# Performance work log

Hardware: AMD Instinct MI355X
Metric: run time of the kernel (lower is better)

The kernel has to match this reference:

```python
import jax, jax.numpy as jnp
import numpy as np

L, D, H, HK, DH, F, V, T, B = 8, 1024, 16, 4, 64, 2816, 32000, 1024, 2
G = H // HK
THETA = 10000.0
EPS = 1e-6
SCALE = DH ** -0.5


def _rope_tables(t, dh, theta):
    inv = 1.0 / theta ** (jnp.arange(0, dh, 2, dtype=jnp.float32) / dh)  # [dh/2]
    ang = jnp.arange(t, dtype=jnp.float32)[:, None] * inv[None, :]       # [T, dh/2]
    return jnp.cos(ang), jnp.sin(ang)


def _apply_rope(x, cos, sin):
    # x: [B, T, h, DH] -> rotate pairs (even, odd)
    xr = x.reshape(*x.shape[:-1], DH // 2, 2)
    x0, x1 = xr[..., 0], xr[..., 1]
    c = cos[None, :, None, :]
    s = sin[None, :, None, :]
    out = jnp.stack([x0 * c - x1 * s, x0 * s + x1 * c], axis=-1)
    return out.reshape(*x.shape)


def _rmsnorm(x, w):
    var = jnp.mean(x * x, axis=-1, keepdims=True)
    return x * jax.lax.rsqrt(var + EPS) * w


def setup_inputs() -> dict:
    key = jax.random.key(0)
    ks = jax.random.split(key, 10)
    s = 0.02
    return {
        "ids": jax.random.randint(ks[0], (B, T), 0, V),
        "emb": jax.random.normal(ks[1], (V, D), jnp.float32) * s,
        "qw": jax.random.normal(ks[2], (L, H * DH, D), jnp.float32) * s,
        "kw": jax.random.normal(ks[3], (L, HK * DH, D), jnp.float32) * s,
        "vw": jax.random.normal(ks[4], (L, HK * DH, D), jnp.float32) * s,
        "ow": jax.random.normal(ks[5], (L, D, D), jnp.float32) * s,
        "w1": jax.random.normal(ks[6], (L, F, D), jnp.float32) * s,
        "w2": jax.random.normal(ks[7], (L, D, F), jnp.float32) * s,
        "w3": jax.random.normal(ks[8], (L, F, D), jnp.float32) * s,
        "n1": jnp.ones((L, D), jnp.float32),
        "n2": jnp.ones((L, D), jnp.float32),
        "nf": jnp.ones((D,), jnp.float32),
    }


def _forward(ids, emb, qw, kw, vw, ow, w1, w2, w3, n1, n2, nf):
    cos, sin = _rope_tables(T, DH, THETA)
    causal = jnp.tril(jnp.ones((T, T), dtype=bool))  # [T, T]
    x = emb[ids]  # [B, T, D]
    for l in range(L):
        xn = _rmsnorm(x, n1[l])
        q = jnp.einsum("btd,ed->bte", xn, qw[l]).reshape(B, T, H, DH)
        k = jnp.einsum("btd,ed->bte", xn, kw[l]).reshape(B, T, HK, DH)
        v = jnp.einsum("btd,ed->bte", xn, vw[l]).reshape(B, T, HK, DH)
        q = _apply_rope(q, cos, sin)
        k = _apply_rope(k, cos, sin)
        # GQA: group query heads over shared kv heads
        qg = q.transpose(0, 2, 1, 3).reshape(B, HK, G, T, DH)
        kh = k.transpose(0, 2, 1, 3)  # [B, HK, T, DH]
        vh = v.transpose(0, 2, 1, 3)
        scores = jnp.einsum("bkgtd,bksd->bkgts", qg, kh) * SCALE
        scores = jnp.where(causal, scores, -jnp.inf)
        p = jax.nn.softmax(scores, axis=-1)
        out = jnp.einsum("bkgts,bksd->bkgtd", p, vh)
        out = out.reshape(B, H, T, DH).transpose(0, 2, 1, 3).reshape(B, T, D)
        x = x + jnp.einsum("btd,ed->bte", out, ow[l])
        xn2 = _rmsnorm(x, n2[l])
        h1 = jnp.einsum("btd,fd->btf", xn2, w1[l])
        h3 = jnp.einsum("btd,fd->btf", xn2, w3[l])
        x = x + jnp.einsum("btf,df->btd", jax.nn.silu(h1) * h3, w2[l])
    x = _rmsnorm(x, nf)
    logits = jnp.einsum("btd,vd->btv", x, emb)  # tied lm_head
    return logits


def reference(ids, emb, qw, kw, vw, ow, w1, w2, w3, n1, n2, nf):
    return _forward(ids, emb, qw, kw, vw, ow, w1, w2, w3, n1, n2, nf)
```

## Files before the change

### kernel.cpp

```cpp
#include <hip/hip_runtime.h>
#include <math.h>

#define L_ 8
#define D_ 1024
#define H_ 16
#define HK_ 4
#define DH_ 64
#define F_ 2816
#define V_ 32000
#define T_ 1024
#define B_ 2
#define M_ (B_*T_)
#define SCALE_ 0.125f

typedef unsigned short u16;
typedef unsigned int   u32;
typedef __attribute__((ext_vector_type(4))) float  f32x4;
typedef __attribute__((ext_vector_type(8))) short  bf16x8;
typedef __attribute__((ext_vector_type(4))) unsigned short u16x4;
typedef __attribute__((ext_vector_type(4))) unsigned int   u32x4;

__device__ __forceinline__ float bf2f(u16 h) {
    union { u32 u; float f; } v; v.u = ((u32)h) << 16; return v.f;
}
__device__ __forceinline__ u16 f2bf(float f) {
    union { float f; u32 u; } v; v.f = f;
    u32 r = v.u + 0x7fffu + ((v.u >> 16) & 1u);
    return (u16)(r >> 16);
}

__device__ __forceinline__ void gl_lds16(const void* g, void* l) {
    __builtin_amdgcn_global_load_lds(
        (const __attribute__((address_space(1))) unsigned int*)g,
        (__attribute__((address_space(3))) unsigned int*)l,
        16, 0, 0);
}

template<int BM, int BN, int EPI>
__global__ __launch_bounds__(256)
void gemm2_k(const u16* __restrict__ A, int K,
             const u16* __restrict__ W, int N,
             float* __restrict__ Of, u16* __restrict__ Ob,
             const float* __restrict__ tc, const float* __restrict__ ts)
{
    constexpr int FM = BM / 32;
    constexpr int FN = BN / 32;
    constexpr int GM = M_ / BM;
    constexpr int IPA = BM / 64;
    constexpr int IPB = BN / 64;
    __shared__ u16 sA[2 * BM * 32];
    __shared__ u16 sB[2 * BN * 32];

    const int tid  = threadIdx.x;
    const int lane = tid & 63, wv = tid >> 6;
    const int wm = wv >> 1, wn = wv & 1;
    const int l15 = lane & 15, lhi = lane >> 4;
    const int m0 = wm * (BM / 2), n0 = wn * (BN / 2);

    const int nwg = gridDim.x;
    const int q8 = nwg >> 3, r8 = nwg & 7;
    const int xcd = blockIdx.x & 7, off8 = blockIdx.x >> 3;
    const int wgid = (xcd < r8 ? xcd * (q8 + 1) : r8 * (q8 + 1) + (xcd - r8) * q8) + off8;
    const int tM = wgid % GM, tN = wgid / GM;

    const int srow = lane >> 2;
    const int scol = (lane & 3) * 8;

    const u16* Abase = A + (size_t)(tM * BM) * K;
    const u16* Wbase = W + (size_t)(tN * BN) * K;

    f32x4 acc[FM][FN];
#pragma unroll
    for (int i = 0; i < FM; ++i)
#pragma unroll
        for (int j = 0; j < FN; ++j) acc[i][j] = f32x4{0.f, 0.f, 0.f, 0.f};

    auto stage = [&](int kt, int buf) {
        u16* sa = sA + buf * (BM * 32);
        u16* sb = sB + buf * (BN * 32);
#pragma unroll
        for (int i = 0; i < IPA; ++i) {
            int c = wv * IPA + i;
            gl_lds16(Abase + (size_t)(c * 16 + srow) * K + kt + scol, sa + c * 512);
        }
#pragma unroll
        for (int i = 0; i < IPB; ++i) {
            int c = wv * IPB + i;
            gl_lds16(Wbase + (size_t)(c * 16 + srow) * K + kt + scol, sb + c * 512);
        }
    };

    const int nt = K >> 5;
    stage(0, 0);
    asm volatile("s_waitcnt vmcnt(0)" ::: "memory");
    __syncthreads();

    int cur = 0;
    for (int t = 0; t < nt; ++t) {
        if (t + 1 < nt) stage((t + 1) << 5, cur ^ 1);

        const u16* sa = sA + cur * (BM * 32);
        const u16* sb = sB + cur * (BN * 32);
        bf16x8 av[FM], bv[FN];
#pragma unroll
        for (int i = 0; i < FM; ++i)
            av[i] = *(const bf16x8*)&sa[(m0 + i * 16 + l15) * 32 + lhi * 8];
#pragma unroll
        for (int j = 0; j < FN; ++j)
            bv[j] = *(const bf16x8*)&sb[(n0 + j * 16 + l15) * 32 + lhi * 8];
#pragma unroll
        for (int i = 0; i < FM; ++i)
#pragma unroll
            for (int j = 0; j < FN; ++j)
                acc[i][j] = __builtin_amdgcn_mfma_f32_16x16x32_bf16(
                    av[i], bv[j], acc[i][j], 0, 0, 0);

        if (t + 1 < nt) {
            asm volatile("s_waitcnt vmcnt(0)" ::: "memory");
            __syncthreads();
            cur ^= 1;
        }
    }

#pragma unroll
    for (int i = 0; i < FM; ++i)
#pragma unroll
        for (int j = 0; j < FN; ++j) {
            size_t gm = (size_t)tM * BM + m0 + i * 16 + lhi * 4;
            size_t gn = (size_t)tN * BN + n0 + j * 16 + l15;
#pragma unroll
            for (int r = 0; r < 4; ++r) {
                float v = acc[i][j][r];
                size_t idx = (gm + r) * (size_t)N + gn;
                if (EPI == 0) {
                    Ob[idx] = f2bf(v);
                } else if (EPI == 1) {
                    Of[idx] = v;
                } else if (EPI == 2) {
                    Of[idx] += v;
                } else if (EPI == 3) {
                    float b = __shfl_xor(v, 1);
                    if ((lane & 1) == 0) {
                        float s = v / (1.0f + expf(-v));
                        Ob[(gm + r) * (size_t)F_ + (gn >> 1)] = f2bf(s * b);
                    }
                } else {
                    float b = __shfl_xor(v, 1);
                    int gni = (int)gn;
                    int gmr = (int)(gm + r);
                    if (gni < 1280) {
                        int dd = gni & 63;
                        int jj = dd >> 1;
                        int tt = gmr & (T_ - 1);
                        float c = tc[tt * 32 + jj], s = ts[tt * 32 + jj];
                        float ro = ((dd & 1) == 0) ? (v * c - b * s) : (b * s + v * c);
                        Ob[idx] = f2bf(ro);
                    } else {
                        int vc = gni - 1280;
                        int hk = vc >> 6, dd = vc & 63;
                        int bb = gmr >> 10, tt = gmr & (T_ - 1);
                        ((u16*)Of)[((size_t)((bb * HK_ + hk) * DH_ + dd)) * T_ + tt] = f2bf(v);
                    }
                }
            }
        }
}

__global__ __launch_bounds__(256)
void cvt_k(const float* __restrict__ src, u16* __restrict__ dst,
           unsigned long long sStride, unsigned long long dStride)
{
    int l = blockIdx.y;
    size_t i = ((size_t)blockIdx.x * 256 + threadIdx.x) * 4;
    f32x4 v = *(const f32x4*)(src + l * sStride + i);
    u16x4 o;
    o.x = f2bf(v.x); o.y = f2bf(v.y); o.z = f2bf(v.z); o.w = f2bf(v.w);
    *(u16x4*)(dst + l * dStride + i) = o;
}

__global__ __launch_bounds__(256)
void cvt_il_k(const float* __restrict__ src, u16* __restrict__ dst,
              unsigned long long sStride, unsigned long long dStride, int off)
{
    int f = blockIdx.x, l = blockIdx.y;
    int i = threadIdx.x * 4;
    f32x4 v = *(const f32x4*)(src + l * sStride + (size_t)f * D_ + i);
    u16x4 o;
    o.x = f2bf(v.x); o.y = f2bf(v.y); o.z = f2bf(v.z); o.w = f2bf(v.w);
    *(u16x4*)(dst + l * dStride + (size_t)(2 * f + off) * D_ + i) = o;
}

template<int BM, int BN, int EPI, int NW>
__global__ __launch_bounds__(256)
void gemm_k(const u16* __restrict__ A, int K,
            const float* __restrict__ W0, const float* __restrict__ W1p,
            const float* __restrict__ W2p, int N0, int N1, int N,
            float* __restrict__ Of, u16* __restrict__ Ob)
{
    constexpr int FM = BM / 32;
    constexpr int FN = BN / 32;
    constexpr int LS = 40;
    __shared__ u16 sA[BM * LS];
    __shared__ u16 sB[BN * LS];

    const int tid  = threadIdx.x;
    const int lane = tid & 63, wv = tid >> 6;
    const int wm = wv >> 1, wn = wv & 1;
    const int l15 = lane & 15, lhi = lane >> 4;
    const int m0 = wm * (BM / 2), n0 = wn * (BN / 2);
    const int tM = blockIdx.y, tN = blockIdx.x;

    f32x4 acc[FM][FN];
#pragma unroll
    for (int i = 0; i < FM; ++i)
#pragma unroll
        for (int j = 0; j < FN; ++j) acc[i][j] = f32x4{0.f, 0.f, 0.f, 0.f};

    for (int kt = 0; kt < K; kt += 32) {
#pragma unroll
        for (int i = 0; i < BM / 64; ++i) {
            int cid = tid + i * 256;
            int row = cid >> 2, kc = cid & 3;
            const u16* src = A + (size_t)(tM * BM + row) * K + kt + kc * 8;
            *(u32x4*)&sA[row * LS + kc * 8] = *(const u32x4*)src;
        }
#pragma unroll
        for (int i = 0; i < BN / 32; ++i) {
            int cid = tid + i * 256;
            int row = cid >> 3, kc = cid & 7;
            int n = tN * BN + row;
            const float* wr;
            if (NW == 1)      wr = W0 + (size_t)n * K;
            else if (NW == 2) wr = (n < N0) ? (W0 + (size_t)n * K)
                                            : (W1p + (size_t)(n - N0) * K);
            else              wr = (n < N0) ? (W0 + (size_t)n * K)
                               : (n < N0 + N1) ? (W1p + (size_t)(n - N0) * K)
                                               : (W2p + (size_t)(n - N0 - N1) * K);
            f32x4 v = *(const f32x4*)(wr + kt + kc * 4);
            u16x4 o;
            o.x = f2bf(v.x); o.y = f2bf(v.y); o.z = f2bf(v.z); o.w = f2bf(v.w);
            *(u16x4*)&sB[row * LS + kc * 4] = o;
        }
        __syncthreads();

        bf16x8 av[FM], bv[FN];
#pragma unroll
        for (int i = 0; i < FM; ++i)
            av[i] = *(const bf16x8*)&sA[(m0 + i * 16 + l15) * LS + lhi * 8];
#pragma unroll
        for (int j = 0; j < FN; ++j)
            bv[j] = *(const bf16x8*)&sB[(n0 + j * 16 + l15) * LS + lhi * 8];
#pragma unroll
        for (int i = 0; i < FM; ++i)
#pragma unroll
            for (int j = 0; j < FN; ++j)
                acc[i][j] = __builtin_amdgcn_mfma_f32_16x16x32_bf16(
                    av[i], bv[j], acc[i][j], 0, 0, 0);
        __syncthreads();
    }

#pragma unroll
    for (int i = 0; i < FM; ++i)
#pragma unroll
        for (int j = 0; j < FN; ++j) {
            size_t gm = (size_t)tM * BM + m0 + i * 16 + lhi * 4;
            size_t gn = (size_t)tN * BN + n0 + j * 16 + l15;
#pragma unroll
            for (int r = 0; r < 4; ++r) {
                float v = acc[i][j][r];
                size_t idx = (gm + r) * (size_t)N + gn;
                if (EPI == 0)      Ob[idx] = f2bf(v);
                else if (EPI == 1) Of[idx] = v;
                else               Of[idx] += v;
            }
        }
}

__global__ __launch_bounds__(512)
void attn3_k(const u16* __restrict__ qkv, const u16* __restrict__ vt,
             u16* __restrict__ attn)
{
    const int qt = 31 - blockIdx.x;
    const int hk = blockIdx.y, b = blockIdx.z;
    const int tid = threadIdx.x;
    const int lane = tid & 63, w = tid >> 6;
    const int l15 = lane & 15, lhi = lane >> 4;
    const int h = hk * 4 + (w & 3);
    const int rg = w >> 2;

    __shared__ u16 sK[128 * 64];
    __shared__ u16 sVT[64 * 128];
    __shared__ u16 sP[8][16 * 136];

    const int q0 = qt * 32;
    const int qr0 = q0 + rg * 16;
    const u16* qptr = qkv + (size_t)(b * T_ + qr0 + l15) * 1536 + h * 64 + lhi * 8;
    bf16x8 aq0 = *(const bf16x8*)qptr;
    bf16x8 aq1 = *(const bf16x8*)(qptr + 32);

    f32x4 accO[4];
#pragma unroll
    for (int d = 0; d < 4; ++d) accO[d] = f32x4{0.f, 0.f, 0.f, 0.f};
    float m_r[4] = {-1e30f, -1e30f, -1e30f, -1e30f};
    float l_r[4] = {0.f, 0.f, 0.f, 0.f};
    const int myq = qr0 + lhi * 4;
    const int qmaxw = qr0 + 15;
    u16* sPw = sP[w];

    const int ntiles = (qt >> 2) + 1;
    const u16* vtb = vt + (size_t)((b * HK_ + hk) * DH_) * T_;
    const int L = lane;

    for (int kt = 0; kt < ntiles; ++kt) {
        const int t0 = kt * 128;
#pragma unroll
        for (int i = 0; i < 2; ++i) {
            int c = w * 2 + i;
            int row = c * 8 + (L >> 3);
            int p = L & 7;
            const u16* src = qkv + (size_t)(b * T_ + t0 + row) * 1536 + 1024 + hk * 64
                             + ((p ^ (row & 7)) * 8);
            gl_lds16(src, sK + c * 512);
        }
#pragma unroll
        for (int i = 0; i < 2; ++i) {
            int c = w * 2 + i;
            int row = c * 4 + (L >> 4);
            int p = L & 15;
            const u16* src = vtb + (size_t)row * T_ + t0 + ((p ^ (row & 15)) * 8);
            gl_lds16(src, sVT + c * 512);
        }
        asm volatile("s_waitcnt vmcnt(0)" ::: "memory");
        __syncthreads();

        const bool lastt = (kt == ntiles - 1);

        f32x4 accS[8];
#pragma unroll
        for (int nf = 0; nf < 8; ++nf)
            accS[nf] = f32x4{-1e30f, -1e30f, -1e30f, -1e30f};
#pragma unroll
        for (int pk = 0; pk < 4; ++pk) {
            if (t0 + pk * 32 > qmaxw) continue;
            f32x4 s0 = f32x4{0.f, 0.f, 0.f, 0.f};
            f32x4 s1 = f32x4{0.f, 0.f, 0.f, 0.f};
#pragma unroll
            for (int kk = 0; kk < 2; ++kk) {
                bf16x8 aqs = kk ? aq1 : aq0;
                int r0 = (pk * 2) * 16 + l15;
                int r1 = (pk * 2 + 1) * 16 + l15;
                int ls = kk * 4 + lhi;
                bf16x8 b0 = *(const bf16x8*)&sK[r0 * 64 + ((ls ^ (r0 & 7)) * 8)];
                bf16x8 b1 = *(const bf16x8*)&sK[r1 * 64 + ((ls ^ (r1 & 7)) * 8)];
                s0 = __builtin_amdgcn_mfma_f32_16x16x32_bf16(aqs, b0, s0, 0, 0, 0);
                s1 = __builtin_amdgcn_mfma_f32_16x16x32_bf16(aqs, b1, s1, 0, 0, 0);
            }
#pragma unroll
            for (int r = 0; r < 4; ++r) {
                float v0 = s0[r] * SCALE_;
                float v1 = s1[r] * SCALE_;
                if (lastt) {
                    int kp0 = t0 + (pk * 2) * 16 + l15;
                    int kp1 = kp0 + 16;
                    if (kp0 > myq + r) v0 = -1e30f;
                    if (kp1 > myq + r) v1 = -1e30f;
                }
                accS[pk * 2][r] = v0;
                accS[pk * 2 + 1][r] = v1;
            }
        }

        float sc[4];
#pragma unroll
        for (int r = 0; r < 4; ++r) {
            float mx = accS[0][r];
#pragma unroll
            for (int nf = 1; nf < 8; ++nf) mx = fmaxf(mx, accS[nf][r]);
#pragma unroll
            for (int off = 1; off < 16; off <<= 1) mx = fmaxf(mx, __shfl_xor(mx, off));
            float mn = fmaxf(m_r[r], mx);
            sc[r] = expf(m_r[r] - mn);
            m_r[r] = mn;
        }
        float rs[4] = {0.f, 0.f, 0.f, 0.f};
#pragma unroll
        for (int pk = 0; pk < 4; ++pk) {
            if (t0 + pk * 32 > qmaxw) continue;
#pragma unroll
            for (int g = 0; g < 2; ++g) {
                int nf = pk * 2 + g;
#pragma unroll
                for (int r = 0; r < 4; ++r) {
                    float p = expf(accS[nf][r] - m_r[r]);
                    accS[nf][r] = p;
                    rs[r] += p;
                }
            }
        }
#pragma unroll
        for (int r = 0; r < 4; ++r) {
#pragma unroll
            for (int off = 1; off < 16; off <<= 1) rs[r] += __shfl_xor(rs[r], off);
            l_r[r] = l_r[r] * sc[r] + rs[r];
        }
#pragma unroll
        for (int d = 0; d < 4; ++d)
#pragma unroll
            for (int r = 0; r < 4; ++r) accO[d][r] *= sc[r];

#pragma unroll
        for (int pk = 0; pk < 4; ++pk) {
            if (t0 + pk * 32 > qmaxw) continue;
#pragma unroll
            for (int g = 0; g < 2; ++g) {
                int nf = pk * 2 + g;
#pragma unroll
                for (int r = 0; r < 4; ++r)
                    sPw[(lhi * 4 + r) * 136 + nf * 16 + l15] = f2bf(accS[nf][r]);
            }
        }

#pragma unroll
        for (int kk = 0; kk < 4; ++kk) {
            if (t0 + kk * 32 > qmaxw) continue;
            bf16x8 pas = *(const bf16x8*)&sPw[l15 * 136 + kk * 32 + lhi * 8];
#pragma unroll
            for (int nf = 0; nf < 4; ++nf) {
                int row = nf * 16 + l15;
                int ls = kk * 4 + lhi;
                bf16x8 bvv = *(const bf16x8*)&sVT[row * 128 + ((ls ^ (row & 15)) * 8)];
                accO[nf] = __builtin_amdgcn_mfma_f32_16x16x32_bf16(pas, bvv, accO[nf], 0, 0, 0);
            }
        }
        __syncthreads();
    }

#pragma unroll
    for (int d = 0; d < 4; ++d)
#pragma unroll
        for (int r = 0; r < 4; ++r) {
            int row = qr0 + lhi * 4 + r;
            float o = accO[d][r] / l_r[r];
            attn[(size_t)(b * T_ + row) * 1024 + h * 64 + d * 16 + l15] = f2bf(o);
        }
}

__global__ __launch_bounds__(256)
void attn_k(const u16* __restrict__ qkv, u16* __restrict__ attn)
{
    const int qt = blockIdx.x, h = blockIdx.y, b = blockIdx.z;
    const int hk = h >> 2;
    const int tid = threadIdx.x;
    const int lane = tid & 63, w = tid >> 6;
    const int l15 = lane & 15, lhi = lane >> 4;
    __shared__ u16 sK[64 * 72];
    __shared__ u16 sVT[64 * 74];
    __shared__ u16 sP[4 * 16 * 72];

    const int q0 = qt * 64;
    const u16* qptr = qkv + (size_t)(b * T_ + q0 + w * 16 + l15) * 1536 + h * 64 + lhi * 8;
    bf16x8 aq0 = *(const bf16x8*)qptr;
    bf16x8 aq1 = *(const bf16x8*)(qptr + 32);

    f32x4 accO[4];
#pragma unroll
    for (int d = 0; d < 4; ++d) accO[d] = f32x4{0.f, 0.f, 0.f, 0.f};
    float m_r[4] = {-1e30f, -1e30f, -1e30f, -1e30f};
    float l_r[4] = {0.f, 0.f, 0.f, 0.f};
    const int myq = q0 + w * 16 + lhi * 4;
    u16* sPw = sP + w * 16 * 72;

    for (int kt = 0; kt <= qt; ++kt) {
#pragma unroll
        for (int i = 0; i < 2; ++i) {
            int cid = tid + i * 256;
            int r = cid >> 3, kc = cid & 7;
            const u16* src = qkv + (size_t)(b * T_ + kt * 64 + r) * 1536 + 1024 + hk * 64 + kc * 8;
            *(u32x4*)&sK[r * 72 + kc * 8] = *(const u32x4*)src;
        }
#pragma unroll
        for (int i = 0; i < 2; ++i) {
            int cid = tid + i * 256;
            int tt = cid >> 3, dc = cid & 7;
            const u16* src = qkv + (size_t)(b * T_ + kt * 64 + tt) * 1536 + 1280 + hk * 64 + dc * 8;
            bf16x8 vv = *(const bf16x8*)src;
#pragma unroll
            for (int j = 0; j < 8; ++j) sVT[(dc * 8 + j) * 74 + tt] = (u16)vv[j];
        }
        __syncthreads();

        f32x4 accS[4];
#pragma unroll
        for (int nf = 0; nf < 4; ++nf) accS[nf] = f32x4{0.f, 0.f, 0.f, 0.f};
#pragma unroll
        for (int s = 0; s < 2; ++s) {
            bf16x8 aqs = s ? aq1 : aq0;
#pragma unroll
            for (int nf = 0; nf < 4; ++nf) {
                bf16x8 bk = *(const bf16x8*)&sK[(nf * 16 + l15) * 72 + s * 32 + lhi * 8];
                accS[nf] = __builtin_amdgcn_mfma_f32_16x16x32_bf16(aqs, bk, accS[nf], 0, 0, 0);
            }
        }
#pragma unroll
        for (int nf = 0; nf < 4; ++nf)
#pragma unroll
            for (int r = 0; r < 4; ++r) {
                float v = accS[nf][r] * SCALE_;
                if (kt == qt) {
                    int kp = kt * 64 + nf * 16 + l15;
                    if (kp > myq + r) v = -1e30f;
                }
                accS[nf][r] = v;
            }
        float sc[4];
#pragma unroll
        for (int r = 0; r < 4; ++r) {
            float mx = fmaxf(fmaxf(accS[0][r], accS[1][r]), fmaxf(accS[2][r], accS[3][r]));
#pragma unroll
            for (int off = 1; off < 16; off <<= 1) mx = fmaxf(mx, __shfl_xor(mx, off));
            float mn = fmaxf(m_r[r], mx);
            sc[r] = expf(m_r[r] - mn);
            m_r[r] = mn;
        }
        float rs[4] = {0.f, 0.f, 0.f, 0.f};
#pragma unroll
        for (int nf = 0; nf < 4; ++nf)
#pragma unroll
            for (int r = 0; r < 4; ++r) {
                float p = expf(accS[nf][r] - m_r[r]);
                accS[nf][r] = p;
                rs[r] += p;
            }
#pragma unroll
        for (int r = 0; r < 4; ++r) {
#pragma unroll
            for (int off = 1; off < 16; off <<= 1) rs[r] += __shfl_xor(rs[r], off);
            l_r[r] = l_r[r] * sc[r] + rs[r];
        }
#pragma unroll
        for (int d = 0; d < 4; ++d)
#pragma unroll
            for (int r = 0; r < 4; ++r) accO[d][r] *= sc[r];

#pragma unroll
        for (int nf = 0; nf < 4; ++nf)
#pragma unroll
            for (int r = 0; r < 4; ++r)
                sPw[(lhi * 4 + r) * 72 + nf * 16 + l15] = f2bf(accS[nf][r]);
        bf16x8 pa0 = *(const bf16x8*)&sPw[l15 * 72 + lhi * 8];
        bf16x8 pa1 = *(const bf16x8*)&sPw[l15 * 72 + 32 + lhi * 8];
#pragma unroll
        for (int s = 0; s < 2; ++s) {
            bf16x8 pas = s ? pa1 : pa0;
#pragma unroll
            for (int d = 0; d < 4; ++d) {
                bf16x8 bvv = *(const bf16x8*)&sVT[(d * 16 + l15) * 74 + s * 32 + lhi * 8];
                accO[d] = __builtin_amdgcn_mfma_f32_16x16x32_bf16(pas, bvv, accO[d], 0, 0, 0);
            }
        }
        __syncthreads();
    }

#pragma unroll
    for (int d = 0; d < 4; ++d)
#pragma unroll
        for (int r = 0; r < 4; ++r) {
            int row = q0 + w * 16 + lhi * 4 + r;
            float o = accO[d][r] / l_r[r];
            attn[(size_t)(b * T_ + row) * 1024 + h * 64 + d * 16 + l15] = f2bf(o);
        }
}

__global__ __launch_bounds__(256)
void gather_k(const int* __restrict__ ids, const float* __restrict__ emb,
              float* __restrict__ x)
{
    int m = blockIdx.x, tid = threadIdx.x;
    int id = ids[m];
    *(f32x4*)(x + (size_t)m * D_ + tid * 4) =
        *(const f32x4*)(emb + (size_t)id * D_ + tid * 4);
}

__global__ __launch_bounds__(256)
void rmsnorm_k(const float* __restrict__ x, const float* __restrict__ g,
               u16* __restrict__ out)
{
    const int row = blockIdx.x, tid = threadIdx.x;
    const float* xr = x + (size_t)row * D_;
    f32x4 v = *(const f32x4*)(xr + tid * 4);
    float ss = v.x * v.x + v.y * v.y + v.z * v.z + v.w * v.w;
#pragma unroll
    for (int off = 32; off >= 1; off >>= 1) ss += __shfl_xor(ss, off);
    __shared__ float red[4];
    if ((tid & 63) == 0) red[tid >> 6] = ss;
    __syncthreads();
    float tot = red[0] + red[1] + red[2] + red[3];
    float rr = rsqrtf(tot * (1.0f / D_) + 1e-6f);
    f32x4 wv = *(const f32x4*)(g + tid * 4);
    u16x4 o;
    o.x = f2bf(v.x * rr * wv.x); o.y = f2bf(v.y * rr * wv.y);
    o.z = f2bf(v.z * rr * wv.z); o.w = f2bf(v.w * rr * wv.w);
    *(u16x4*)(out + (size_t)row * D_ + tid * 4) = o;
}

__global__ __launch_bounds__(256)
void rope_tab_k(float* __restrict__ tc, float* __restrict__ ts)
{
    int idx = blockIdx.x * 256 + threadIdx.x;
    int t = idx >> 5, j = idx & 31;
    float inv = powf(10000.0f, -(float)j * (1.0f / 32.0f));
    float ang = (float)t * inv;
    tc[idx] = cosf(ang);
    ts[idx] = sinf(ang);
}

__global__ __launch_bounds__(256)
void silu_f32_k(const float* __restrict__ h13, u16* __restrict__ hh)
{
    int m = blockIdx.y;
    int f = blockIdx.x * 256 + threadIdx.x;
    float a = h13[(size_t)m * (2 * F_) + f];
    float c = h13[(size_t)m * (2 * F_) + F_ + f];
    float s = a / (1.0f + expf(-a));
    hh[(size_t)m * F_ + f] = f2bf(s * c);
}

__global__ __launch_bounds__(640)
void rope_slow_k(u16* __restrict__ qkv)
{
    int m = blockIdx.x;
    int c2 = threadIdx.x;
    int col = (c2 < 512) ? (c2 * 2) : (1024 + (c2 - 512) * 2);
    int d = col & 63;
    int t = m & (T_ - 1);
    float ang = (float)t * powf(10000.0f, -(float)d / 64.0f);
    float cs = cosf(ang), sn = sinf(ang);
    u16* p = qkv + (size_t)m * 1536 + col;
    float x0 = bf2f(p[0]), x1 = bf2f(p[1]);
    p[0] = f2bf(x0 * cs - x1 * sn);
    p[1] = f2bf(x0 * sn + x1 * cs);
}

extern "C" void kernel_launch(void* const* d_in, const int* in_sizes, int n_in,
                              void* d_out, int out_size, void* d_ws, size_t ws_size,
                              hipStream_t stream)
{
    const int*   ids = (const int*)d_in[0];
    const float* emb = (const float*)d_in[1];
    const float* qw  = (const float*)d_in[2];
    const float* kw  = (const float*)d_in[3];
    const float* vw  = (const float*)d_in[4];
    const float* ow  = (const float*)d_in[5];
    const float* w1  = (const float*)d_in[6];
    const float* w2  = (const float*)d_in[7];
    const float* w3  = (const float*)d_in[8];
    const float* n1  = (const float*)d_in[9];
    const float* n2  = (const float*)d_in[10];
    const float* nfw = (const float*)d_in[11];
    float* out = (float*)d_out;
    char*  ws  = (char*)d_ws;

    float* x    = (float*)(ws);
    u16*   xn   = (u16*)(ws + 8388608ULL);
    u16*   qkvb = (u16*)(ws + 12582912ULL);
    u16*   attnb= (u16*)(ws + 18874368ULL);
    u16*   hh   = (u16*)(ws + 46137344ULL);
    float* ropec= (float*)(ws + 57671680ULL);
    float* ropes= (float*)(ws + 57802752ULL);
    u16*   embb = (u16*)(ws + 57933824ULL);
    u16*   wqkv = (u16*)(ws + 123469824ULL);
    u16*   wob  = (u16*)(ws + 148635648ULL);
    u16*   w13b = (u16*)(ws + 165412864ULL);
    u16*   w2b  = (u16*)(ws + 257687552ULL);
    u16*   vtb  = (u16*)(ws + 303824896ULL);
    const unsigned long long NEED = 304873472ULL;

    if (ws_size >= NEED) {
        cvt_k<<<dim3(32000, 1), 256, 0, stream>>>(emb, embb, 0, 0);
        cvt_k<<<dim3(1024, L_), 256, 0, stream>>>(qw, wqkv,            1048576ULL, 1572864ULL);
        cvt_k<<<dim3(256,  L_), 256, 0, stream>>>(kw, wqkv + 1048576,  262144ULL,  1572864ULL);
        cvt_k<<<dim3(256,  L_), 256, 0, stream>>>(vw, wqkv + 1310720,  262144ULL,  1572864ULL);
        cvt_k<<<dim3(1024, L_), 256, 0, stream>>>(ow, wob,             1048576ULL, 1048576ULL);
        cvt_il_k<<<dim3(2816, L_), 256, 0, stream>>>(w1, w13b, 2883584ULL, 5767168ULL, 0);
        cvt_il_k<<<dim3(2816, L_), 256, 0, stream>>>(w3, w13b, 2883584ULL, 5767168ULL, 1);
        cvt_k<<<dim3(2816, L_), 256, 0, stream>>>(w2, w2b,             2883584ULL, 2883584ULL);
        rope_tab_k<<<T_ * 32 / 256, 256, 0, stream>>>(ropec, ropes);

        gather_k<<<M_, 256, 0, stream>>>(ids, emb, x);

        for (int l = 0; l < L_; ++l) {
            rmsnorm_k<<<M_, 256, 0, stream>>>(x, n1 + l * D_, xn);
            gemm2_k<64, 64, 4><<<32 * 24, 256, 0, stream>>>(
                xn, D_, wqkv + (size_t)l * 1572864, 1536, (float*)vtb, qkvb, ropec, ropes);
            attn3_k<<<dim3(32, HK_, B_), 512, 0, stream>>>(qkvb, vtb, attnb);
            gemm2_k<64, 64, 2><<<32 * 16, 256, 0, stream>>>(
                attnb, D_, wob + (size_t)l * 1048576, 1024, x, nullptr, nullptr, nullptr);
            rmsnorm_k<<<M_, 256, 0, stream>>>(x, n2 + l * D_, xn);
            gemm2_k<128, 128, 3><<<16 * 44, 256, 0, stream>>>(
                xn, D_, w13b + (size_t)l * 5767168, 5632, nullptr, hh, nullptr, nullptr);
            gemm2_k<64, 64, 2><<<32 * 16, 256, 0, stream>>>(
                hh, F_, w2b + (size_t)l * 2883584, 1024, x, nullptr, nullptr, nullptr);
        }

        rmsnorm_k<<<M_, 256, 0, stream>>>(x, nfw, xn);
        gemm2_k<128, 128, 1><<<16 * 250, 256, 0, stream>>>(
            xn, D_, embb, V_, out, nullptr, nullptr, nullptr);
        return;
    }

    float* h13f = (float*)(ws + 23068672ULL);
    u16*   hhf  = (u16*)(ws + 69206016ULL);
    gather_k<<<M_, 256, 0, stream>>>(ids, emb, x);

    for (int l = 0; l < L_; ++l) {
        rmsnorm_k<<<M_, 256, 0, stream>>>(x, n1 + l * D_, xn);
        gemm_k<128, 64, 0, 3><<<dim3(24, 16), 256, 0, stream>>>(
            xn, D_,
            qw + (size_t)l * H_ * DH_ * D_,
            kw + (size_t)l * HK_ * DH_ * D_,
            vw + (size_t)l * HK_ * DH_ * D_,
            1024, 256, 1536, nullptr, qkvb);
        rope_slow_k<<<M_, 640, 0, stream>>>(qkvb);
        attn_k<<<dim3(T_ / 64, H_, B_), 256, 0, stream>>>(qkvb, attnb);
        gemm_k<128, 64, 2, 1><<<dim3(16, 16), 256, 0, stream>>>(
            attnb, D_, ow + (size_t)l * D_ * D_, nullptr, nullptr,
            0, 0, D_, x, nullptr);
        rmsnorm_k<<<M_, 256, 0, stream>>>(x, n2 + l * D_, xn);
        gemm_k<128, 128, 1, 2><<<dim3(44, 16), 256, 0, stream>>>(
            xn, D_, w1 + (size_t)l * F_ * D_, w3 + (size_t)l * F_ * D_, nullptr,
            F_, 0, 2 * F_, h13f, nullptr);
        silu_f32_k<<<dim3(11, M_), 256, 0, stream>>>(h13f, hhf);
        gemm_k<128, 64, 2, 1><<<dim3(16, 16), 256, 0, stream>>>(
            hhf, F_, w2 + (size_t)l * D_ * F_, nullptr, nullptr,
            0, 0, D_, x, nullptr);
    }

    rmsnorm_k<<<M_, 256, 0, stream>>>(x, nfw, xn);
    gemm_k<128, 128, 1, 1><<<dim3(250, 16), 256, 0, stream>>>(
        xn, D_, emb, nullptr, nullptr, 0, 0, V_, out, nullptr);
}
```

Baseline: 1.807 ms.

## Add 256x256-tile 8-wave GEMM kernel for FFN up-projection and LM head

Adds a new 512-thread GEMM kernel with 256x256 output tiles, XOR-swizzled LDS staging via direct global-to-LDS loads, a double-buffered A/B pipeline with loads spread across sub-phases, XCD-aware block remapping, and raised wave priority around MFMA bursts. It replaces the 128x128 gemm2_k for the fused W1/W3 SwiGLU projection and the tied LM-head projection. The aim is more reuse per loaded tile and better overlap of memory with MFMA work. In exchange it uses a large LDS footprint and many accumulators, and launches far fewer workgroups (176 for the FFN), which may underfill the GPU.

```diff
diff --git a/kernel.cpp b/kernel.cpp
--- a/kernel.cpp
+++ b/kernel.cpp
@@ -34,6 +34,149 @@
         (const __attribute__((address_space(1))) unsigned int*)g,
         (__attribute__((address_space(3))) unsigned int*)l,
         16, 0, 0);
+}
+
+__device__ __forceinline__ void bar8() {
+    asm volatile("" ::: "memory");
+    __builtin_amdgcn_s_barrier();
+    asm volatile("" ::: "memory");
+}
+
+template<int EPI>
+__global__ __launch_bounds__(512)
+void gemm8_k(const u16* __restrict__ A, int K,
+             const u16* __restrict__ W, int N,
+             float* __restrict__ Of, u16* __restrict__ Ob)
+{
+    constexpr int TS = 256 * 64;
+    __shared__ u16 sA[2 * TS];
+    __shared__ u16 sB[2 * TS];
+
+    const int tid = threadIdx.x;
+    const int lane = tid & 63, wv = tid >> 6;
+    const int wm = wv >> 2, wn = wv & 3;
+    const int l15 = lane & 15, lhi = lane >> 4;
+
+    const int nwg = gridDim.x;
+    const int q8 = nwg >> 3;
+    const int xcd = blockIdx.x & 7, off8 = blockIdx.x >> 3;
+    const int wgid = xcd * q8 + off8;
+    const int tM = wgid & 7, tN = wgid >> 3;
+
+    const u16* Abase = A + (size_t)(tM * 256) * K;
+    const u16* Wbase = W + (size_t)(tN * 256) * K;
+
+    const int srow8 = lane >> 3;
+    const int sp    = lane & 7;
+    const int scol  = (sp ^ srow8) * 8;
+
+    auto stage = [&](const u16* gbase, int t2, int h, u16* dst) {
+        const u16* g = gbase + (size_t)(h * 128) * K + (t2 << 6);
+        u16* d = dst + h * 8192;
+#pragma unroll
+        for (int i = 0; i < 2; ++i) {
+            int c = wv * 2 + i;
+            int row = c * 8 + srow8;
+            gl_lds16(g + (size_t)row * K + scol, d + c * 512);
+        }
+    };
+
+    f32x4 acc[8][4];
+#pragma unroll
+    for (int i = 0; i < 8; ++i)
+#pragma unroll
+        for (int j = 0; j < 4; ++j) acc[i][j] = f32x4{0.f, 0.f, 0.f, 0.f};
+
+    const int nt = K >> 6;
+    stage(Abase, 0, 0, sA); stage(Abase, 0, 1, sA);
+    stage(Wbase, 0, 0, sB); stage(Wbase, 0, 1, sB);
+    if (nt > 1) {
+        stage(Wbase, 1, 0, sB + TS); stage(Wbase, 1, 1, sB + TS);
+        asm volatile("s_waitcnt vmcnt(4)" ::: "memory");
+    } else {
+        asm volatile("s_waitcnt vmcnt(0)" ::: "memory");
+    }
+    bar8();
+
+    for (int t = 0; t < nt; ++t) {
+        const int cur = t & 1;
+        const u16* sa = sA + cur * TS;
+        const u16* sb = sB + cur * TS;
+        u16* saN = sA + (cur ^ 1) * TS;
+        u16* sbN = sB + cur * TS;
+
+        bf16x8 breg[4][2];
+
+#pragma unroll
+        for (int p = 0; p < 4; ++p) {
+            if (p == 0) {
+#pragma unroll
+                for (int j = 0; j < 4; ++j)
+#pragma unroll
+                    for (int kk = 0; kk < 2; ++kk) {
+                        int br = wn * 64 + j * 16 + l15;
+                        int ls = kk * 4 + lhi;
+                        breg[j][kk] = *(const bf16x8*)
+                            &sb[br * 64 + ((ls ^ (br & 7)) * 8)];
+                    }
+            }
+            bf16x8 areg[2][2];
+#pragma unroll
+            for (int mi = 0; mi < 2; ++mi)
+#pragma unroll
+                for (int kk = 0; kk < 2; ++kk) {
+                    int ar = wm * 128 + (p * 2 + mi) * 16 + l15;
+                    int ls = kk * 4 + lhi;
+                    areg[mi][kk] = *(const bf16x8*)
+                        &sa[ar * 64 + ((ls ^ (ar & 7)) * 8)];
+                }
+
+            if (p == 0 && t + 1 < nt) stage(Abase, t + 1, 0, saN);
+            if (p == 1 && t + 1 < nt) stage(Abase, t + 1, 1, saN);
+            if (p == 2 && t + 2 < nt) stage(Wbase, t + 2, 0, sbN);
+            if (p == 3 && t + 2 < nt) stage(Wbase, t + 2, 1, sbN);
+
+            if (p == 3 && t + 1 < nt) {
+                if (t + 2 < nt) asm volatile("s_waitcnt vmcnt(4)" ::: "memory");
+                else            asm volatile("s_waitcnt vmcnt(0)" ::: "memory");
+            }
+
+            bar8();
+            asm volatile("s_waitcnt lgkmcnt(0)" ::: "memory");
+            __builtin_amdgcn_s_setprio(1);
+#pragma unroll
+            for (int mi = 0; mi < 2; ++mi)
+#pragma unroll
+                for (int j = 0; j < 4; ++j)
+#pragma unroll
+                    for (int kk = 0; kk < 2; ++kk)
+                        acc[p * 2 + mi][j] = __builtin_amdgcn_mfma_f32_16x16x32_bf16(
+                            areg[mi][kk], breg[j][kk], acc[p * 2 + mi][j], 0, 0, 0);
+            __builtin_amdgcn_s_setprio(0);
+            bar8();
+        }
+    }
+
+#pragma unroll
+    for (int i = 0; i < 8; ++i)
+#pragma unroll
+        for (int j = 0; j < 4; ++j) {
+            size_t gm = (size_t)tM * 256 + wm * 128 + i * 16 + lhi * 4;
+            size_t gn = (size_t)tN * 256 + wn * 64 + j * 16 + l15;
+#pragma unroll
+            for (int r = 0; r < 4; ++r) {
+                float v = acc[i][j][r];
+                if (EPI == 1) {
+                    Of[(gm + r) * (size_t)N + gn] = v;
+                } else {
+                    float b = __shfl_xor(v, 1);
+                    if ((lane & 1) == 0) {
+                        float s = v / (1.0f + expf(-v));
+                        Ob[(gm + r) * (size_t)F_ + (gn >> 1)] = f2bf(s * b);
+                    }
+                }
+            }
+        }
 }
 
 template<int BM, int BN, int EPI>
@@ -696,15 +839,15 @@
             gemm2_k<64, 64, 2><<<32 * 16, 256, 0, stream>>>(
                 attnb, D_, wob + (size_t)l * 1048576, 1024, x, nullptr, nullptr, nullptr);
             rmsnorm_k<<<M_, 256, 0, stream>>>(x, n2 + l * D_, xn);
-            gemm2_k<128, 128, 3><<<16 * 44, 256, 0, stream>>>(
-                xn, D_, w13b + (size_t)l * 5767168, 5632, nullptr, hh, nullptr, nullptr);
+            gemm8_k<3><<<8 * 22, 512, 0, stream>>>(
+                xn, D_, w13b + (size_t)l * 5767168, 5632, nullptr, hh);
             gemm2_k<64, 64, 2><<<32 * 16, 256, 0, stream>>>(
                 hh, F_, w2b + (size_t)l * 2883584, 1024, x, nullptr, nullptr, nullptr);
         }
 
         rmsnorm_k<<<M_, 256, 0, stream>>>(x, nfw, xn);
-        gemm2_k<128, 128, 1><<<16 * 250, 256, 0, stream>>>(
-            xn, D_, embb, V_, out, nullptr, nullptr, nullptr);
+        gemm8_k<1><<<8 * 125, 512, 0, stream>>>(
+            xn, D_, embb, V_, out, nullptr);
         return;
     }
 
```

Result: slower. 1.950 ms (+7.9%).
